# Kernel optimization log

Measured on AMD Instinct MI355X. Metric: run time of the kernel, lower is better.

## Reference

```python
import jax, jax.numpy as jnp
import numpy as np

WCD, WCOV, WQUAL = 1.0, 1e-4, 1e-4
BIG = 1e10  # penalty to exclude zero-rows from min/argmin


def _calus(x, y):
    # x: [B, N, 3], y: [B, M, 3]
    B, N, _ = x.shape
    M = y.shape[1]
    # _remove_zero_rows filters rows whose coordinate SUM is zero -> mask instead
    mx = x.sum(-1) != 0  # [B, N] valid x points
    my = y.sum(-1) != 0  # [B, M] valid y points
    dt = x.dtype
    # squared pairwise distances d[b, j, i] = ||x[b,i] - y[b,j]||^2  (expanded form)
    xn = jnp.sum(x * x, axis=-1)  # [B, N]
    yn = jnp.sum(y * y, axis=-1)  # [B, M]
    d = yn[:, :, None] + xn[:, None, :] - 2.0 * jnp.einsum('bmc,bnc->bmn', y, x)  # [B, M, N]
    # push invalid rows/cols out of every min
    d = d + jnp.where(mx, 0.0, BIG).astype(dt)[:, None, :] \
          + jnp.where(my, 0.0, BIG).astype(dt)[:, :, None]
    x_min = jnp.min(d, axis=1)     # [B, N] nearest-y distance per x point
    x_arg = jnp.argmin(d, axis=1)  # [B, N] index into y
    y_min = jnp.min(d, axis=2)     # [B, M] nearest-x distance per y point
    y_arg = jnp.argmin(d, axis=2)  # [B, M] index into x
    fmx, fmy = mx.astype(dt), my.astype(dt)
    nx, ny = fmx.sum(-1), fmy.sum(-1)  # valid counts per sample
    # chamfer = mean over x-points + mean over y-points (torch cat+sum)
    cd = jnp.sum(x_min * fmx, -1) / nx + jnp.sum(y_min * fmy, -1) / ny  # [B]
    # coverage: fraction of y indices hit by some valid x point (unique count)
    rows = jnp.arange(B)[:, None]
    hit_y = jnp.zeros((B, M), dt).at[rows, x_arg].max(fmx)
    cov = hit_y.sum(-1) / ny  # [B]
    # quality: fraction of x indices hit by some valid y point
    hit_x = jnp.zeros((B, N), dt).at[rows, y_arg].max(fmy)
    qual = hit_x.sum(-1) / nx  # [B]
    return cd.mean(), cov.mean(), qual.mean()


def setup_inputs() -> dict:
    key = jax.random.key(0)
    kx, ky = jax.random.split(key)
    B, N, M = 32, 2048, 2048
    x = jax.random.normal(kx, (B, N, 3), dtype=jnp.float32)
    y = jax.random.normal(ky, (B, M, 3), dtype=jnp.float32)
    return {"x": x, "y": y}


def reference(x, y):
    cd, cov, qual = _calus(x, y)
    val = WCD * cd - WCOV * cov - WQUAL * qual
    return (val, cd, cov, qual)
```

## Files before the change

### kernel.cpp

```cpp
#include <hip/hip_runtime.h>
#include <stdint.h>


#define BB 32
#define NP 2048
#define BIGF 1e10f

typedef unsigned int u32;

__device__ __forceinline__ float emb_min(float best, float d, u32 jg) {
  u32 bits = (__float_as_uint(d) & 0xFFFFF800u) | jg;
  return fminf(best, __uint_as_float(bits));
}

__global__ __launch_bounds__(512) void nn_fused_kernel(
    const float* __restrict__ x, const float* __restrict__ y,
    u32* __restrict__ hitmask, float* __restrict__ sums,
    float* __restrict__ cnts) {
  int bid = blockIdx.x;
  int side = bid >> 8;
  int b = (bid >> 3) & 31;
  int pc = bid & 7;

  __shared__ float4 qs[NP + 8];
  __shared__ u32 merged[8][256];
  __shared__ float pxn[256];
  __shared__ float pvalid[256];

  int tid = threadIdx.x;
  const float* qraw = (side ? x : y) + b * NP * 3;
  for (int k = 0; k < 4; ++k) {
    int i = tid + 512 * k;
    float q0 = qraw[3 * i], q1 = qraw[3 * i + 1], q2 = qraw[3 * i + 2];
    float s = q0 + q1 + q2;
    float qn = q0 * q0 + q1 * q1 + q2 * q2;
    if (s == 0.0f) qn += BIGF;
    qs[i] = make_float4(-2.0f * q0, -2.0f * q1, -2.0f * q2, qn);
  }

  int w = tid >> 6, lane = tid & 63;
  const float* praw = (side ? y : x) + (b * NP + pc * 256) * 3;
  float p0[4], p1[4], p2[4];
  for (int k = 0; k < 4; ++k) {
    int pl = lane + 64 * k;
    p0[k] = praw[3 * pl];
    p1[k] = praw[3 * pl + 1];
    p2[k] = praw[3 * pl + 2];
    if (w == 0) {
      pxn[pl] = p0[k] * p0[k] + p1[k] * p1[k] + p2[k] * p2[k];
      pvalid[pl] = ((p0[k] + p1[k] + p2[k]) != 0.0f) ? 1.0f : 0.0f;
    }
  }
  __syncthreads();

  float best0 = 3.0e38f, best1 = 3.0e38f, best2 = 3.0e38f, best3 = 3.0e38f;
  const float4* qq = &qs[w * 256];
  u32 qoff = (u32)(w * 256);

#define PROC(q, jg)                                                              \
  {                                                                              \
    float d0 = fmaf((q).x, p0[0], fmaf((q).y, p1[0], fmaf((q).z, p2[0], (q).w))); \
    float d1 = fmaf((q).x, p0[1], fmaf((q).y, p1[1], fmaf((q).z, p2[1], (q).w))); \
    float d2 = fmaf((q).x, p0[2], fmaf((q).y, p1[2], fmaf((q).z, p2[2], (q).w))); \
    float d3 = fmaf((q).x, p0[3], fmaf((q).y, p1[3], fmaf((q).z, p2[3], (q).w))); \
    best0 = emb_min(best0, d0, (jg));                                            \
    best1 = emb_min(best1, d1, (jg));                                            \
    best2 = emb_min(best2, d2, (jg));                                            \
    best3 = emb_min(best3, d3, (jg));                                            \
  }

  float4 qa0 = qq[0], qa1 = qq[1], qa2 = qq[2], qa3 = qq[3];
  for (int jc = 0; jc < 256; jc += 8) {
    float4 qb0 = qq[jc + 4], qb1 = qq[jc + 5], qb2 = qq[jc + 6], qb3 = qq[jc + 7];
    u32 jg = qoff + (u32)jc;
    PROC(qa0, jg);     PROC(qa1, jg + 1); PROC(qa2, jg + 2); PROC(qa3, jg + 3);
    qa0 = qq[jc + 8];  qa1 = qq[jc + 9];  qa2 = qq[jc + 10]; qa3 = qq[jc + 11];
    PROC(qb0, jg + 4); PROC(qb1, jg + 5); PROC(qb2, jg + 6); PROC(qb3, jg + 7);
  }

  merged[w][lane +   0] = __float_as_uint(best0);
  merged[w][lane +  64] = __float_as_uint(best1);
  merged[w][lane + 128] = __float_as_uint(best2);
  merged[w][lane + 192] = __float_as_uint(best3);
  __syncthreads();

  float contrib = 0.f, cnt = 0.f;
  if (tid < 256) {
    float bd = __uint_as_float(merged[0][tid]);
    for (int ww = 1; ww < 8; ++ww)
      bd = fminf(bd, __uint_as_float(merged[ww][tid]));
    u32 bits = __float_as_uint(bd);
    u32 bi = bits & 0x7FFu;
    float dmin = __uint_as_float(bits & 0xFFFFF800u);
    float valid = pvalid[tid];
    contrib = valid * (dmin + pxn[tid]);
    cnt = valid;
    if (valid != 0.0f)
      atomicOr(&hitmask[(side * BB + b) * 64 + (bi >> 5)], 1u << (bi & 31));
  }
  for (int o = 32; o > 0; o >>= 1) {
    contrib += __shfl_down(contrib, o, 64);
    cnt += __shfl_down(cnt, o, 64);
  }
  if (lane == 0 && w < 4) {
    atomicAdd(&sums[side * BB + b], contrib);
    atomicAdd(&cnts[side * BB + b], cnt);
  }
}

__global__ __launch_bounds__(64) void assemble_kernel(const u32* __restrict__ hitmask,
                                                      const float* __restrict__ sums,
                                                      const float* __restrict__ cnts,
                                                      float* __restrict__ out) {
  int t = threadIdx.x;
  float cd = 0.f, cov = 0.f, qual = 0.f;
  if (t < BB) {
    float nx = cnts[t], ny = cnts[BB + t];
    int hy = 0, hx = 0;
    for (int i = 0; i < 64; ++i) hy += __popc(hitmask[t * 64 + i]);
    for (int i = 0; i < 64; ++i) hx += __popc(hitmask[(BB + t) * 64 + i]);
    cd = sums[t] / nx + sums[BB + t] / ny;
    cov = (float)hy / ny;
    qual = (float)hx / nx;
  }
  for (int o = 32; o > 0; o >>= 1) {
    cd += __shfl_down(cd, o, 64);
    cov += __shfl_down(cov, o, 64);
    qual += __shfl_down(qual, o, 64);
  }
  if (t == 0) {
    cd /= (float)BB; cov /= (float)BB; qual /= (float)BB;
    out[0] = cd - 1e-4f * cov - 1e-4f * qual;
    out[1] = cd;
    out[2] = cov;
    out[3] = qual;
  }
}

extern "C" void kernel_launch(void* const* d_in, const int* in_sizes, int n_in,
                              void* d_out, int out_size, void* d_ws, size_t ws_size,
                              hipStream_t stream) {
  const float* x = (const float*)d_in[0];
  const float* y = (const float*)d_in[1];
  float* out = (float*)d_out;
  char* ws = (char*)d_ws;

  u32* hitmask = (u32*)ws;
  float* sums = (float*)(ws + 16384);
  float* cnts = sums + 2 * BB;

  hipMemsetAsync(ws, 0, 16384 + 512, stream);
  nn_fused_kernel<<<2 * BB * 8, 512, 0, stream>>>(x, y, hitmask, sums, cnts);
  assemble_kernel<<<1, 64, 0, stream>>>(hitmask, sums, cnts, out);
}
```

Baseline: 91.75 us.

## Pre-pack points into float4 buffer, read queries from global, drop atomics and memset

Adds a pack kernel that converts both point clouds into float4 (xyz, norm plus invalid penalty) once. The NN kernel now streams query points directly from global memory instead of staging 2048 points per block in LDS, so each block no longer reloads and preprocesses the query set. Global atomics and the memset are replaced by per-block partial sums and hit masks, which a wider assemble kernel combines. The inner loop pairs min operations. This adds a kernel launch and depends on cache hits for the repeated global query reads.

```diff
diff --git a/kernel.cpp b/kernel.cpp
--- a/kernel.cpp
+++ b/kernel.cpp
@@ -4,78 +4,81 @@
 
 #define BB 32
 #define NP 2048
+#define NPTS (BB * NP)
 #define BIGF 1e10f
 
 typedef unsigned int u32;
 
-__device__ __forceinline__ float emb_min(float best, float d, u32 jg) {
-  u32 bits = (__float_as_uint(d) & 0xFFFFF800u) | jg;
-  return fminf(best, __uint_as_float(bits));
+__global__ __launch_bounds__(256) void pack_kernel(const float* __restrict__ x,
+                                                   const float* __restrict__ y,
+                                                   float4* __restrict__ pk) {
+  int t = blockIdx.x * 256 + threadIdx.x;
+  int side = t >> 16;
+  int i = t & (NPTS - 1);
+  const float* src = side ? y : x;
+  float v0 = src[3 * i], v1 = src[3 * i + 1], v2 = src[3 * i + 2];
+  float vn = v0 * v0 + v1 * v1 + v2 * v2;
+  if (v0 + v1 + v2 == 0.0f) vn += BIGF;
+  pk[t] = make_float4(v0, v1, v2, vn);
 }
 
-__global__ __launch_bounds__(512) void nn_fused_kernel(
-    const float* __restrict__ x, const float* __restrict__ y,
-    u32* __restrict__ hitmask, float* __restrict__ sums,
-    float* __restrict__ cnts) {
+#define EMB(d, jg) __uint_as_float((__float_as_uint(d) & 0xFFFFF800u) | (u32)(jg))
+
+__global__ __launch_bounds__(512) void nn_kernel(const float4* __restrict__ pk,
+                                                 u32* __restrict__ hitpart,
+                                                 float* __restrict__ sums_part,
+                                                 float* __restrict__ cnts_part) {
   int bid = blockIdx.x;
   int side = bid >> 8;
   int b = (bid >> 3) & 31;
   int pc = bid & 7;
+  int tid = threadIdx.x;
+  int w = __builtin_amdgcn_readfirstlane(tid >> 6);
+  int lane = tid & 63;
 
-  __shared__ float4 qs[NP + 8];
   __shared__ u32 merged[8][256];
-  __shared__ float pxn[256];
-  __shared__ float pvalid[256];
+  __shared__ float pws[256];
+  __shared__ u32 hitlds[64];
+  __shared__ float redc[8], redn[8];
 
-  int tid = threadIdx.x;
-  const float* qraw = (side ? x : y) + b * NP * 3;
+  const float4* pbase = pk + side * NPTS + b * NP + pc * 256;
+  float pmx[4], pmy[4], pmz[4];
   for (int k = 0; k < 4; ++k) {
-    int i = tid + 512 * k;
-    float q0 = qraw[3 * i], q1 = qraw[3 * i + 1], q2 = qraw[3 * i + 2];
-    float s = q0 + q1 + q2;
-    float qn = q0 * q0 + q1 * q1 + q2 * q2;
-    if (s == 0.0f) qn += BIGF;
-    qs[i] = make_float4(-2.0f * q0, -2.0f * q1, -2.0f * q2, qn);
+    float4 p = pbase[lane + 64 * k];
+    pmx[k] = -2.0f * p.x; pmy[k] = -2.0f * p.y; pmz[k] = -2.0f * p.z;
+    if (w == 0) pws[lane + 64 * k] = p.w;
   }
+  if (tid < 64) hitlds[tid] = 0u;
 
-  int w = tid >> 6, lane = tid & 63;
-  const float* praw = (side ? y : x) + (b * NP + pc * 256) * 3;
-  float p0[4], p1[4], p2[4];
-  for (int k = 0; k < 4; ++k) {
-    int pl = lane + 64 * k;
-    p0[k] = praw[3 * pl];
-    p1[k] = praw[3 * pl + 1];
-    p2[k] = praw[3 * pl + 2];
-    if (w == 0) {
-      pxn[pl] = p0[k] * p0[k] + p1[k] * p1[k] + p2[k] * p2[k];
-      pvalid[pl] = ((p0[k] + p1[k] + p2[k]) != 0.0f) ? 1.0f : 0.0f;
-    }
-  }
-  __syncthreads();
+  const float4* qq = pk + (side ^ 1) * NPTS + b * NP + w * 256;
+  u32 qoff = (u32)(w * 256);
+  float best0 = 3.0e38f, best1 = 3.0e38f, best2 = 3.0e38f, best3 = 3.0e38f;
 
-  float best0 = 3.0e38f, best1 = 3.0e38f, best2 = 3.0e38f, best3 = 3.0e38f;
-  const float4* qq = &qs[w * 256];
-  u32 qoff = (u32)(w * 256);
-
-#define PROC(q, jg)                                                              \
-  {                                                                              \
-    float d0 = fmaf((q).x, p0[0], fmaf((q).y, p1[0], fmaf((q).z, p2[0], (q).w))); \
-    float d1 = fmaf((q).x, p0[1], fmaf((q).y, p1[1], fmaf((q).z, p2[1], (q).w))); \
-    float d2 = fmaf((q).x, p0[2], fmaf((q).y, p1[2], fmaf((q).z, p2[2], (q).w))); \
-    float d3 = fmaf((q).x, p0[3], fmaf((q).y, p1[3], fmaf((q).z, p2[3], (q).w))); \
-    best0 = emb_min(best0, d0, (jg));                                            \
-    best1 = emb_min(best1, d1, (jg));                                            \
-    best2 = emb_min(best2, d2, (jg));                                            \
-    best3 = emb_min(best3, d3, (jg));                                            \
+#define PROC2(qA, qB, jg)                                                          \
+  {                                                                                \
+    float a0 = fmaf((qA).x, pmx[0], fmaf((qA).y, pmy[0], fmaf((qA).z, pmz[0], (qA).w))); \
+    float a1 = fmaf((qA).x, pmx[1], fmaf((qA).y, pmy[1], fmaf((qA).z, pmz[1], (qA).w))); \
+    float a2 = fmaf((qA).x, pmx[2], fmaf((qA).y, pmy[2], fmaf((qA).z, pmz[2], (qA).w))); \
+    float a3 = fmaf((qA).x, pmx[3], fmaf((qA).y, pmy[3], fmaf((qA).z, pmz[3], (qA).w))); \
+    float b0 = fmaf((qB).x, pmx[0], fmaf((qB).y, pmy[0], fmaf((qB).z, pmz[0], (qB).w))); \
+    float b1 = fmaf((qB).x, pmx[1], fmaf((qB).y, pmy[1], fmaf((qB).z, pmz[1], (qB).w))); \
+    float b2 = fmaf((qB).x, pmx[2], fmaf((qB).y, pmy[2], fmaf((qB).z, pmz[2], (qB).w))); \
+    float b3 = fmaf((qB).x, pmx[3], fmaf((qB).y, pmy[3], fmaf((qB).z, pmz[3], (qB).w))); \
+    best0 = fminf(fminf(best0, EMB(a0, jg)), EMB(b0, (jg) + 1));                   \
+    best1 = fminf(fminf(best1, EMB(a1, jg)), EMB(b1, (jg) + 1));                   \
+    best2 = fminf(fminf(best2, EMB(a2, jg)), EMB(b2, (jg) + 1));                   \
+    best3 = fminf(fminf(best3, EMB(a3, jg)), EMB(b3, (jg) + 1));                   \
   }
 
   float4 qa0 = qq[0], qa1 = qq[1], qa2 = qq[2], qa3 = qq[3];
   for (int jc = 0; jc < 256; jc += 8) {
     float4 qb0 = qq[jc + 4], qb1 = qq[jc + 5], qb2 = qq[jc + 6], qb3 = qq[jc + 7];
     u32 jg = qoff + (u32)jc;
-    PROC(qa0, jg);     PROC(qa1, jg + 1); PROC(qa2, jg + 2); PROC(qa3, jg + 3);
-    qa0 = qq[jc + 8];  qa1 = qq[jc + 9];  qa2 = qq[jc + 10]; qa3 = qq[jc + 11];
-    PROC(qb0, jg + 4); PROC(qb1, jg + 5); PROC(qb2, jg + 6); PROC(qb3, jg + 7);
+    PROC2(qa0, qa1, jg);
+    PROC2(qa2, qa3, jg + 2);
+    qa0 = qq[jc + 8]; qa1 = qq[jc + 9]; qa2 = qq[jc + 10]; qa3 = qq[jc + 11];
+    PROC2(qb0, qb1, jg + 4);
+    PROC2(qb2, qb3, jg + 6);
   }
 
   merged[w][lane +   0] = __float_as_uint(best0);
@@ -87,53 +90,77 @@
   float contrib = 0.f, cnt = 0.f;
   if (tid < 256) {
     float bd = __uint_as_float(merged[0][tid]);
-    for (int ww = 1; ww < 8; ++ww)
-      bd = fminf(bd, __uint_as_float(merged[ww][tid]));
+#pragma unroll
+    for (int ww = 1; ww < 8; ++ww) bd = fminf(bd, __uint_as_float(merged[ww][tid]));
     u32 bits = __float_as_uint(bd);
     u32 bi = bits & 0x7FFu;
     float dmin = __uint_as_float(bits & 0xFFFFF800u);
-    float valid = pvalid[tid];
-    contrib = valid * (dmin + pxn[tid]);
-    cnt = valid;
-    if (valid != 0.0f)
-      atomicOr(&hitmask[(side * BB + b) * 64 + (bi >> 5)], 1u << (bi & 31));
+    float pwv = pws[tid];
+    bool valid = (pwv < 1e9f);
+    contrib = valid ? (dmin + pwv) : 0.f;
+    cnt = valid ? 1.f : 0.f;
+    if (valid) atomicOr(&hitlds[bi >> 5], 1u << (bi & 31));
   }
   for (int o = 32; o > 0; o >>= 1) {
     contrib += __shfl_down(contrib, o, 64);
     cnt += __shfl_down(cnt, o, 64);
   }
-  if (lane == 0 && w < 4) {
-    atomicAdd(&sums[side * BB + b], contrib);
-    atomicAdd(&cnts[side * BB + b], cnt);
+  if (lane == 0 && w < 4) { redc[w] = contrib; redn[w] = cnt; }
+  __syncthreads();
+  if (tid == 0) {
+    sums_part[bid] = redc[0] + redc[1] + redc[2] + redc[3];
+    cnts_part[bid] = redn[0] + redn[1] + redn[2] + redn[3];
   }
+  if (tid < 64) hitpart[bid * 64 + tid] = hitlds[tid];
 }
 
-__global__ __launch_bounds__(64) void assemble_kernel(const u32* __restrict__ hitmask,
-                                                      const float* __restrict__ sums,
-                                                      const float* __restrict__ cnts,
-                                                      float* __restrict__ out) {
-  int t = threadIdx.x;
-  float cd = 0.f, cov = 0.f, qual = 0.f;
-  if (t < BB) {
-    float nx = cnts[t], ny = cnts[BB + t];
-    int hy = 0, hx = 0;
-    for (int i = 0; i < 64; ++i) hy += __popc(hitmask[t * 64 + i]);
-    for (int i = 0; i < 64; ++i) hx += __popc(hitmask[(BB + t) * 64 + i]);
-    cd = sums[t] / nx + sums[BB + t] / ny;
-    cov = (float)hy / ny;
-    qual = (float)hx / nx;
+__global__ __launch_bounds__(512) void assemble_kernel(const u32* __restrict__ hitpart,
+                                                       const float* __restrict__ sums_part,
+                                                       const float* __restrict__ cnts_part,
+                                                       float* __restrict__ out) {
+  __shared__ float hs[64], ss[64], cs[64];
+  int tid = threadIdx.x;
+  int sb = tid >> 3, c = tid & 7;
+  float h = 0.f;
+  for (int wd = c; wd < 64; wd += 8) {
+    u32 m = 0u;
+#pragma unroll
+    for (int blk = 0; blk < 8; ++blk) m |= hitpart[(sb * 8 + blk) * 64 + wd];
+    h += (float)__popc(m);
   }
-  for (int o = 32; o > 0; o >>= 1) {
-    cd += __shfl_down(cd, o, 64);
-    cov += __shfl_down(cov, o, 64);
-    qual += __shfl_down(qual, o, 64);
+  h += __shfl_down(h, 4, 8);
+  h += __shfl_down(h, 2, 8);
+  h += __shfl_down(h, 1, 8);
+  if (c == 0) {
+    float s = 0.f, n = 0.f;
+#pragma unroll
+    for (int blk = 0; blk < 8; ++blk) {
+      s += sums_part[sb * 8 + blk];
+      n += cnts_part[sb * 8 + blk];
+    }
+    hs[sb] = h; ss[sb] = s; cs[sb] = n;
   }
-  if (t == 0) {
-    cd /= (float)BB; cov /= (float)BB; qual /= (float)BB;
-    out[0] = cd - 1e-4f * cov - 1e-4f * qual;
-    out[1] = cd;
-    out[2] = cov;
-    out[3] = qual;
+  __syncthreads();
+  if (tid < 64) {
+    float cd = 0.f, cov = 0.f, qual = 0.f;
+    if (tid < BB) {
+      float nx = cs[tid], ny = cs[BB + tid];
+      cd = ss[tid] / nx + ss[BB + tid] / ny;
+      cov = hs[tid] / ny;
+      qual = hs[BB + tid] / nx;
+    }
+    for (int o = 32; o > 0; o >>= 1) {
+      cd += __shfl_down(cd, o, 64);
+      cov += __shfl_down(cov, o, 64);
+      qual += __shfl_down(qual, o, 64);
+    }
+    if (tid == 0) {
+      cd /= (float)BB; cov /= (float)BB; qual /= (float)BB;
+      out[0] = cd - 1e-4f * cov - 1e-4f * qual;
+      out[1] = cd;
+      out[2] = cov;
+      out[3] = qual;
+    }
   }
 }
 
@@ -145,11 +172,12 @@
   float* out = (float*)d_out;
   char* ws = (char*)d_ws;
 
-  u32* hitmask = (u32*)ws;
-  float* sums = (float*)(ws + 16384);
-  float* cnts = sums + 2 * BB;
+  u32* hitpart = (u32*)ws;
+  float* sums_part = (float*)(ws + 131072);
+  float* cnts_part = (float*)(ws + 133120);
+  float4* pk = (float4*)(ws + 135168);
 
-  hipMemsetAsync(ws, 0, 16384 + 512, stream);
-  nn_fused_kernel<<<2 * BB * 8, 512, 0, stream>>>(x, y, hitmask, sums, cnts);
-  assemble_kernel<<<1, 64, 0, stream>>>(hitmask, sums, cnts, out);
+  pack_kernel<<<2 * NPTS / 256, 256, 0, stream>>>(x, y, pk);
+  nn_kernel<<<2 * BB * 8, 512, 0, stream>>>(pk, hitpart, sums_part, cnts_part);
+  assemble_kernel<<<1, 512, 0, stream>>>(hitpart, sums_part, cnts_part, out);
 }
```

After: 103.4 us. +12.7%, slower.
